# Performance work log

Hardware: AMD Instinct MI355X
Metric: run time of the kernel (lower is better)

Reference implementation:

```python
import jax, jax.numpy as jnp
import numpy as np

DIMS = 512
NUM_HEADS = 8
KEY_DIM = DIMS // NUM_HEADS  # 64
VAL_DIM = DIMS               # 512, shared across heads
B, L = 4, 2048


def setup_inputs() -> dict:
    key = jax.random.key(0)
    ks = jax.random.split(key, 13)
    s = 0.02
    return {
        "query": jax.random.normal(ks[0], (B, L, DIMS), dtype=jnp.float32),
        "key": jax.random.normal(ks[1], (B, L, DIMS), dtype=jnp.float32),
        "value": jax.random.normal(ks[2], (B, L, DIMS), dtype=jnp.float32),
        # linear weights stored as (in, out)
        "Wq": jax.random.normal(ks[3], (DIMS, KEY_DIM * NUM_HEADS), dtype=jnp.float32) * s,
        "bq": jnp.zeros((KEY_DIM * NUM_HEADS,), dtype=jnp.float32),
        "Wk": jax.random.normal(ks[4], (DIMS, KEY_DIM * NUM_HEADS), dtype=jnp.float32) * s,
        "bk": jnp.zeros((KEY_DIM * NUM_HEADS,), dtype=jnp.float32),
        "Wv": jax.random.normal(ks[5], (DIMS, VAL_DIM), dtype=jnp.float32) * s,
        "bv": jnp.zeros((VAL_DIM,), dtype=jnp.float32),
        "Wo": jax.random.normal(ks[6], (VAL_DIM * NUM_HEADS, DIMS), dtype=jnp.float32) * s,
        "bo": jnp.zeros((DIMS,), dtype=jnp.float32),
    }


def reference(query, key, value, Wq, bq, Wk, bk, Wv, bv, Wo, bo):
    b, l, _ = query.shape
    m = key.shape[1]
    q = (query @ Wq + bq).reshape(b, l, KEY_DIM, NUM_HEADS)   # blkh
    k = (key @ Wk + bk).reshape(b, m, KEY_DIM, NUM_HEADS)     # bmkh
    v = value @ Wv + bv                                        # bmv (shared over heads)
    # causal mask: -inf strictly above the diagonal
    mask = jnp.where(jnp.arange(m)[None, :] > jnp.arange(l)[:, None],
                     jnp.float32(-jnp.inf), jnp.float32(0.0))  # [l, m]
    scores = jnp.einsum('blkh,bmkh->bhlm', q, k) + mask
    # original divides (scores+mask) by sqrt(key_dim) before softmax
    attn = jax.nn.softmax(scores / jnp.sqrt(jnp.float32(KEY_DIM)), axis=-1)
    vals = jnp.einsum('bhlm,bmv->blhv', attn, v).reshape(b, l, NUM_HEADS * VAL_DIM)
    return vals @ Wo + bo
```

## Files before the change

kernel.cpp:

```cpp
#include <hip/hip_runtime.h>
#include <hip/hip_bf16.h>


typedef __attribute__((ext_vector_type(8))) short bf16x8;
typedef __attribute__((ext_vector_type(4))) float f32x4;
typedef unsigned short u16;
typedef unsigned int u32;

#define DIMS  512
#define NHEAD 8
#define KDIM  64
#define VDIM  512
#define BATCH 4
#define SEQ   2048
#define ROWS  (BATCH * SEQ)
#define OCOLS (NHEAD * VDIM)

__device__ __forceinline__ u16 f2bf(float x) {
  __hip_bfloat16 b = __float2bfloat16(x);
  u16 u; __builtin_memcpy(&u, &b, 2); return u;
}

__global__ __launch_bounds__(256) void cast_bf16(
    const float* __restrict__ in, u16* __restrict__ out, int n8) {
  int i = blockIdx.x * 256 + threadIdx.x;
  if (i >= n8) return;
  const float4* p = reinterpret_cast<const float4*>(in) + (size_t)i * 2;
  float4 a0 = p[0], a1 = p[1];
  bf16x8 v;
  v[0] = f2bf(a0.x); v[1] = f2bf(a0.y); v[2] = f2bf(a0.z); v[3] = f2bf(a0.w);
  v[4] = f2bf(a1.x); v[5] = f2bf(a1.y); v[6] = f2bf(a1.z); v[7] = f2bf(a1.w);
  reinterpret_cast<bf16x8*>(out)[i] = v;
}

__global__ __launch_bounds__(256) void transpose_to_bf16(
    const float* __restrict__ in, u16* __restrict__ out, int R, int C) {
  __shared__ float t[32][33];
  int tx = threadIdx.x & 31, ty = threadIdx.x >> 5;
  int r0 = blockIdx.y * 32, c0 = blockIdx.x * 32;
  #pragma unroll
  for (int i = 0; i < 32; i += 8)
    t[ty + i][tx] = in[(size_t)(r0 + ty + i) * C + c0 + tx];
  __syncthreads();
  #pragma unroll
  for (int i = 0; i < 32; i += 8) {
    int oc = ty + i;
    out[(size_t)(c0 + oc) * R + r0 + tx] = f2bf(t[tx][oc]);
  }
}

__global__ __launch_bounds__(256) void proj_kernel(
    const u16* __restrict__ Xb, const u16* __restrict__ Wt,
    const float* __restrict__ bias, u16* __restrict__ out,
    int mode, float scale) {
  __shared__ u16 Ct[64][72];
  int lane = threadIdx.x & 63, wave = threadIdx.x >> 6;
  int g = lane >> 4, l15 = lane & 15;
  int row0 = blockIdx.y * 64, cb = blockIdx.x * 64;
  int gr = row0 + wave * 16 + l15;
  f32x4 acc[4] = {};
  for (int k0 = 0; k0 < DIMS; k0 += 32) {
    int ka = k0 + g * 8;
    bf16x8 a = *reinterpret_cast<const bf16x8*>(Xb + (size_t)gr * DIMS + ka);
    #pragma unroll
    for (int c = 0; c < 4; ++c) {
      bf16x8 bfr = *reinterpret_cast<const bf16x8*>(Wt + (size_t)(cb + c * 16 + l15) * DIMS + ka);
      acc[c] = __builtin_amdgcn_mfma_f32_16x16x32_bf16(a, bfr, acc[c], 0, 0, 0);
    }
  }
  #pragma unroll
  for (int c = 0; c < 4; ++c) {
    int col = c * 16 + l15;
    float bi = bias[cb + col];
    #pragma unroll
    for (int r = 0; r < 4; ++r) {
      int rl = wave * 16 + g * 4 + r;
      float v = (acc[c][r] + bi) * scale;
      if (mode == 0) Ct[rl][col] = f2bf(v);
      else           Ct[col][rl] = f2bf(v);
    }
  }
  __syncthreads();
  if (mode == 0) {
    int kd0 = cb >> 3;
    #pragma unroll
    for (int s2 = 0; s2 < 2; ++s2) {
      int seg = threadIdx.x + s2 * 256;
      int l = seg >> 3, h = seg & 7;
      bf16x8 vp;
      #pragma unroll
      for (int j = 0; j < 8; ++j) vp[j] = (short)Ct[l][h + 8 * j];
      int row = row0 + l;
      int b = row >> 11, ll = row & 2047;
      *reinterpret_cast<bf16x8*>(out + (((size_t)(b * NHEAD + h) * SEQ + ll) * KDIM + kd0)) = vp;
    }
  } else {
    int v_ = threadIdx.x >> 2, ch = threadIdx.x & 3;
    int b = row0 >> 11, m0 = row0 & 2047;
    bf16x8 p0, p1;
    #pragma unroll
    for (int j = 0; j < 8; ++j) { p0[j] = (short)Ct[v_][ch * 16 + j]; p1[j] = (short)Ct[v_][ch * 16 + 8 + j]; }
    u16* dst = out + ((size_t)(b * VDIM + cb + v_)) * SEQ + m0 + ch * 16;
    *reinterpret_cast<bf16x8*>(dst) = p0;
    *reinterpret_cast<bf16x8*>(dst + 8) = p1;
  }
}

__global__ __launch_bounds__(256, 3) void attn_kernel(
    const u16* __restrict__ Qp, const u16* __restrict__ Kp,
    const u16* __restrict__ Vt, u16* __restrict__ vals) {
  __shared__ u16 Plds[2][32 * 64];
  __shared__ float Lpart[4][32];
  __shared__ float Rinv[32];
  int lane = threadIdx.x & 63, wave = threadIdx.x >> 6;
  int g = lane >> 4, l15 = lane & 15;
  int wg = blockIdx.x;
  int xcd = wg & 7, idx = wg >> 3;
  int bh = xcd * 4 + (idx & 3);
  int qt = 63 - (idx >> 2);
  int b = bh >> 3, h = bh & 7;
  int q0 = qt * 32;
  const u16* Qh = Qp + (size_t)bh * SEQ * KDIM;
  const u16* Kh = Kp + (size_t)bh * SEQ * KDIM;
  const u16* Vw = Vt + (size_t)b * VDIM * SEQ + (size_t)(wave * 128) * SEQ;

  bf16x8 qa[2][2];
  #pragma unroll
  for (int rf = 0; rf < 2; ++rf)
    #pragma unroll
    for (int ks = 0; ks < 2; ++ks)
      qa[rf][ks] = *reinterpret_cast<const bf16x8*>(
          Qh + (size_t)(q0 + rf * 16 + l15) * KDIM + ks * 32 + g * 8);

  f32x4 acc[2][8] = {};
  float rs[2][4] = {};
  int nt = (qt >> 1) + 1;
  int pcol = wave * 16 + l15;

  auto kload = [&](int t, bf16x8* kb) {
    const u16* base = Kh + (size_t)(t * 64 + wave * 16 + l15) * KDIM;
    kb[0] = *reinterpret_cast<const bf16x8*>(base + g * 8);
    kb[1] = *reinterpret_cast<const bf16x8*>(base + 32 + g * 8);
  };
  auto sphase = [&](int t, bf16x8 kb0, bf16x8 kb1) {
    int m0 = t * 64;
    u16* P = Plds[t & 1];
    f32x4 s[2] = {};
    #pragma unroll
    for (int rf = 0; rf < 2; ++rf) {
      s[rf] = __builtin_amdgcn_mfma_f32_16x16x32_bf16(qa[rf][0], kb0, s[rf], 0, 0, 0);
      s[rf] = __builtin_amdgcn_mfma_f32_16x16x32_bf16(qa[rf][1], kb1, s[rf], 0, 0, 0);
    }
    #pragma unroll
    for (int rf = 0; rf < 2; ++rf)
      #pragma unroll
      for (int r = 0; r < 4; ++r) {
        int prow = rf * 16 + g * 4 + r;
        float p = (m0 + pcol > q0 + prow) ? 0.f : exp2f(s[rf][r]);
        rs[rf][r] += p;
        P[prow * 64 + (pcol ^ ((prow & 7) << 3))] = f2bf(p);
      }
  };

  { bf16x8 kb[2]; kload(0, kb); sphase(0, kb[0], kb[1]); }
  __syncthreads();

  for (int t = 0; t < nt; ++t) {
    int m0 = t * 64;
    const u16* P = Plds[t & 1];
    bool more = (t + 1 < nt);
    bf16x8 kb[2];
    if (more) kload(t + 1, kb);
    #pragma unroll
    for (int ks = 0; ks < 2; ++ks) {
      bf16x8 vb[8];
      #pragma unroll
      for (int c = 0; c < 8; ++c)
        vb[c] = *reinterpret_cast<const bf16x8*>(
            Vw + (size_t)(c * 16 + l15) * SEQ + m0 + ks * 32 + g * 8);
      bf16x8 pa[2];
      #pragma unroll
      for (int ar = 0; ar < 2; ++ar) {
        int qr = ar * 16 + l15;
        pa[ar] = *reinterpret_cast<const bf16x8*>(
            &P[qr * 64 + ((ks * 32 + g * 8) ^ ((qr & 7) << 3))]);
      }
      #pragma unroll
      for (int c = 0; c < 8; ++c)
        #pragma unroll
        for (int ar = 0; ar < 2; ++ar)
          acc[ar][c] = __builtin_amdgcn_mfma_f32_16x16x32_bf16(pa[ar], vb[c], acc[ar][c], 0, 0, 0);
    }
    if (more) sphase(t + 1, kb[0], kb[1]);
    __syncthreads();
  }

  #pragma unroll
  for (int rf = 0; rf < 2; ++rf)
    #pragma unroll
    for (int r = 0; r < 4; ++r) {
      float v = rs[rf][r];
      v += __shfl_xor(v, 1); v += __shfl_xor(v, 2);
      v += __shfl_xor(v, 4); v += __shfl_xor(v, 8);
      rs[rf][r] = v;
    }
  if (l15 == 0) {
    #pragma unroll
    for (int rf = 0; rf < 2; ++rf)
      #pragma unroll
      for (int r = 0; r < 4; ++r)
        Lpart[wave][rf * 16 + g * 4 + r] = rs[rf][r];
  }
  __syncthreads();
  if (threadIdx.x < 32)
    Rinv[threadIdx.x] = 1.0f / (Lpart[0][threadIdx.x] + Lpart[1][threadIdx.x] +
                                Lpart[2][threadIdx.x] + Lpart[3][threadIdx.x]);
  __syncthreads();

  #pragma unroll
  for (int ar = 0; ar < 2; ++ar) {
    #pragma unroll
    for (int c = 0; c < 8; ++c) {
      int vcol = wave * 128 + c * 16 + l15;
      #pragma unroll
      for (int r = 0; r < 4; ++r) {
        int row = ar * 16 + g * 4 + r;
        float o = acc[ar][c][r] * Rinv[row];
        vals[((size_t)(b * SEQ + q0 + row)) * OCOLS + h * VDIM + vcol] = f2bf(o);
      }
    }
  }
}

__global__ __launch_bounds__(256) void out_gemm(
    const u16* __restrict__ vals, const u16* __restrict__ Wot,
    const float* __restrict__ bo, float* __restrict__ out) {
  __shared__ char As[128 * 128];
  __shared__ char Bs[64 * 128];
  int t = threadIdx.x;
  int lane = t & 63, wave = t >> 6;
  int g = lane >> 4, l15 = lane & 15;
  int id = (blockIdx.x & 7) * 64 + (blockIdx.x >> 3);
  int bx = id & 7, by = id >> 3;
  int row0 = by * 128, col0 = bx * 64;
  const int NT = OCOLS / 64;

  auto aglob = [&](int kt, int i) {
    int cid = t + i * 256, r = cid >> 3, ch = cid & 7;
    return *reinterpret_cast<const bf16x8*>(vals + (size_t)(row0 + r) * OCOLS + kt * 64 + ch * 8);
  };
  auto bglob = [&](int kt, int i) {
    int cid = t + i * 256, r = cid >> 3, ch = cid & 7;
    return *reinterpret_cast<const bf16x8*>(Wot + (size_t)(col0 + r) * OCOLS + kt * 64 + ch * 8);
  };
  auto stash = [&](bf16x8* av, bf16x8* bv) {
    #pragma unroll
    for (int i = 0; i < 4; ++i) {
      int cid = t + i * 256, r = cid >> 3, ch = cid & 7;
      *reinterpret_cast<bf16x8*>(As + r * 128 + ((ch * 16) ^ ((r & 7) << 4))) = av[i];
    }
    #pragma unroll
    for (int i = 0; i < 2; ++i) {
      int cid = t + i * 256, r = cid >> 3, ch = cid & 7;
      *reinterpret_cast<bf16x8*>(Bs + r * 128 + ((ch * 16) ^ ((r & 7) << 4))) = bv[i];
    }
  };

  f32x4 acc[2][4] = {};
  bf16x8 av[4], bv[2];
  #pragma unroll
  for (int i = 0; i < 4; ++i) av[i] = aglob(0, i);
  #pragma unroll
  for (int i = 0; i < 2; ++i) bv[i] = bglob(0, i);
  stash(av, bv);
  __syncthreads();

  for (int kt = 0; kt < NT; ++kt) {
    bf16x8 an[4], bn[2];
    if (kt + 1 < NT) {
      #pragma unroll
      for (int i = 0; i < 4; ++i) an[i] = aglob(kt + 1, i);
      #pragma unroll
      for (int i = 0; i < 2; ++i) bn[i] = bglob(kt + 1, i);
    }
    #pragma unroll
    for (int ks = 0; ks < 2; ++ks) {
      bf16x8 af[2];
      #pragma unroll
      for (int rf = 0; rf < 2; ++rf) {
        int row = wave * 32 + rf * 16 + l15;
        af[rf] = *reinterpret_cast<const bf16x8*>(As + row * 128 + ((ks * 64 + g * 16) ^ ((row & 7) << 4)));
      }
      #pragma unroll
      for (int c = 0; c < 4; ++c) {
        int row = c * 16 + l15;
        bf16x8 bfr = *reinterpret_cast<const bf16x8*>(Bs + row * 128 + ((ks * 64 + g * 16) ^ ((row & 7) << 4)));
        #pragma unroll
        for (int rf = 0; rf < 2; ++rf)
          acc[rf][c] = __builtin_amdgcn_mfma_f32_16x16x32_bf16(af[rf], bfr, acc[rf][c], 0, 0, 0);
      }
    }
    __syncthreads();
    if (kt + 1 < NT) {
      stash(an, bn);
      __syncthreads();
    }
  }

  #pragma unroll
  for (int c = 0; c < 4; ++c) {
    int col = col0 + c * 16 + l15;
    float bi = bo[col];
    #pragma unroll
    for (int rf = 0; rf < 2; ++rf)
      #pragma unroll
      for (int r = 0; r < 4; ++r) {
        int row = row0 + wave * 32 + rf * 16 + g * 4 + r;
        out[(size_t)row * DIMS + col] = acc[rf][c][r] + bi;
      }
  }
}

extern "C" void kernel_launch(void* const* d_in, const int* in_sizes, int n_in,
                              void* d_out, int out_size, void* d_ws, size_t ws_size,
                              hipStream_t stream) {
  const float* query = (const float*)d_in[0];
  const float* key   = (const float*)d_in[1];
  const float* value = (const float*)d_in[2];
  const float* Wq    = (const float*)d_in[3];
  const float* bq    = (const float*)d_in[4];
  const float* Wk    = (const float*)d_in[5];
  const float* bk    = (const float*)d_in[6];
  const float* Wv    = (const float*)d_in[7];
  const float* bv    = (const float*)d_in[8];
  const float* Wo    = (const float*)d_in[9];
  const float* bo    = (const float*)d_in[10];
  float* out = (float*)d_out;

  char* ws = (char*)d_ws;
  size_t off = 0;
  auto alloc = [&](size_t bytes) {
    char* p = ws + off; off += (bytes + 255) & ~(size_t)255; return p;
  };
  u16* Wqt  = (u16*)alloc((size_t)512 * 512 * 2);
  u16* Wkt  = (u16*)alloc((size_t)512 * 512 * 2);
  u16* Wvt  = (u16*)alloc((size_t)512 * 512 * 2);
  u16* Wot  = (u16*)alloc((size_t)512 * 4096 * 2);
  u16* Qp   = (u16*)alloc((size_t)BATCH * NHEAD * SEQ * KDIM * 2);
  u16* Kp   = (u16*)alloc((size_t)BATCH * NHEAD * SEQ * KDIM * 2);
  u16* Vt   = (u16*)alloc((size_t)BATCH * VDIM * SEQ * 2);
  u16* vals = (u16*)alloc((size_t)ROWS * OCOLS * 2);
  u16* Xq = vals;
  u16* Xk = vals + (size_t)ROWS * DIMS;
  u16* Xv = vals + (size_t)2 * ROWS * DIMS;

  dim3 tb(256);
  const int N8 = ROWS * DIMS / 8;
  cast_bf16<<<dim3(N8 / 256), tb, 0, stream>>>(query, Xq, N8);
  cast_bf16<<<dim3(N8 / 256), tb, 0, stream>>>(key,   Xk, N8);
  cast_bf16<<<dim3(N8 / 256), tb, 0, stream>>>(value, Xv, N8);

  transpose_to_bf16<<<dim3(16, 16), tb, 0, stream>>>(Wq, Wqt, 512, 512);
  transpose_to_bf16<<<dim3(16, 16), tb, 0, stream>>>(Wk, Wkt, 512, 512);
  transpose_to_bf16<<<dim3(16, 16), tb, 0, stream>>>(Wv, Wvt, 512, 512);
  transpose_to_bf16<<<dim3(16, 128), tb, 0, stream>>>(Wo, Wot, 4096, 512);

  const float qscale = 0.18033688011112042f;
  proj_kernel<<<dim3(8, 128), tb, 0, stream>>>(Xq, Wqt, bq, Qp, 0, qscale);
  proj_kernel<<<dim3(8, 128), tb, 0, stream>>>(Xk, Wkt, bk, Kp, 0, 1.0f);
  proj_kernel<<<dim3(8, 128), tb, 0, stream>>>(Xv, Wvt, bv, Vt, 2, 1.0f);

  attn_kernel<<<dim3(2048), tb, 0, stream>>>(Qp, Kp, Vt, vals);

  out_gemm<<<dim3(512), tb, 0, stream>>>(vals, Wot, bo, out);
}
```

Measured before the change: 604.6 us.

## Widen attention workgroup to 8 waves with 128-key tiles and transposed score MFMA

The attention kernel now runs 512 threads (8 waves), each covering 64 value columns instead of 128, and processes 128 keys per iteration instead of 64. Scores are computed as K·Q^T, so each lane owns one query row and can write four packed bf16 probabilities in one store and keep a single row-sum. Key sub-tiles lying entirely above the causal diagonal on the last tile are zero-filled without doing the MFMA. The aim is fewer loop iterations and barriers, higher occupancy, and less per-lane reduction work. The cost is more LDS per block and partly wasted work on the padded final tile.

```diff
diff --git a/kernel.cpp b/kernel.cpp
--- a/kernel.cpp
+++ b/kernel.cpp
@@ -106,11 +106,11 @@
   }
 }
 
-__global__ __launch_bounds__(256, 3) void attn_kernel(
+__global__ __launch_bounds__(512, 4) void attn_kernel(
     const u16* __restrict__ Qp, const u16* __restrict__ Kp,
     const u16* __restrict__ Vt, u16* __restrict__ vals) {
-  __shared__ u16 Plds[2][32 * 64];
-  __shared__ float Lpart[4][32];
+  __shared__ u16 Plds[2][32 * 128];
+  __shared__ float Lpart[8][32];
   __shared__ float Rinv[32];
   int lane = threadIdx.x & 63, wave = threadIdx.x >> 6;
   int g = lane >> 4, l15 = lane & 15;
@@ -122,71 +122,88 @@
   int q0 = qt * 32;
   const u16* Qh = Qp + (size_t)bh * SEQ * KDIM;
   const u16* Kh = Kp + (size_t)bh * SEQ * KDIM;
-  const u16* Vw = Vt + (size_t)b * VDIM * SEQ + (size_t)(wave * 128) * SEQ;
-
-  bf16x8 qa[2][2];
+  const u16* Vw = Vt + (size_t)b * VDIM * SEQ + (size_t)(wave * 64) * SEQ;
+
+  bf16x8 qb[2][2];
   #pragma unroll
   for (int rf = 0; rf < 2; ++rf)
     #pragma unroll
     for (int ks = 0; ks < 2; ++ks)
-      qa[rf][ks] = *reinterpret_cast<const bf16x8*>(
+      qb[rf][ks] = *reinterpret_cast<const bf16x8*>(
           Qh + (size_t)(q0 + rf * 16 + l15) * KDIM + ks * 32 + g * 8);
 
-  f32x4 acc[2][8] = {};
-  float rs[2][4] = {};
-  int nt = (qt >> 1) + 1;
-  int pcol = wave * 16 + l15;
+  f32x4 acc[2][4] = {};
+  float rs[2] = {0.f, 0.f};
+  int nt = ((q0 + 31) >> 7) + 1;
+  int mrow = wave * 16 + l15;
 
   auto kload = [&](int t, bf16x8* kb) {
-    const u16* base = Kh + (size_t)(t * 64 + wave * 16 + l15) * KDIM;
+    const u16* base = Kh + (size_t)(t * 128 + mrow) * KDIM;
     kb[0] = *reinterpret_cast<const bf16x8*>(base + g * 8);
     kb[1] = *reinterpret_cast<const bf16x8*>(base + 32 + g * 8);
   };
   auto sphase = [&](int t, bf16x8 kb0, bf16x8 kb1) {
-    int m0 = t * 64;
     u16* P = Plds[t & 1];
-    f32x4 s[2] = {};
+    int mbase = t * 128 + wave * 16;
+    bool lastt = (t == nt - 1);
+    if (lastt && (mbase > q0 + 31)) {
+      #pragma unroll
+      for (int rf = 0; rf < 2; ++rf) {
+        int ql = rf * 16 + l15;
+        uint2 z; z.x = 0u; z.y = 0u;
+        *reinterpret_cast<uint2*>(&P[ql * 128 + ((wave * 16 + g * 4) ^ ((ql & 7) << 3))]) = z;
+      }
+      return;
+    }
+    f32x4 st[2] = {};
     #pragma unroll
     for (int rf = 0; rf < 2; ++rf) {
-      s[rf] = __builtin_amdgcn_mfma_f32_16x16x32_bf16(qa[rf][0], kb0, s[rf], 0, 0, 0);
-      s[rf] = __builtin_amdgcn_mfma_f32_16x16x32_bf16(qa[rf][1], kb1, s[rf], 0, 0, 0);
-    }
-    #pragma unroll
-    for (int rf = 0; rf < 2; ++rf)
+      st[rf] = __builtin_amdgcn_mfma_f32_16x16x32_bf16(kb0, qb[rf][0], st[rf], 0, 0, 0);
+      st[rf] = __builtin_amdgcn_mfma_f32_16x16x32_bf16(kb1, qb[rf][1], st[rf], 0, 0, 0);
+    }
+    #pragma unroll
+    for (int rf = 0; rf < 2; ++rf) {
+      int qg = q0 + rf * 16 + l15;
+      u16 pb[4];
       #pragma unroll
       for (int r = 0; r < 4; ++r) {
-        int prow = rf * 16 + g * 4 + r;
-        float p = (m0 + pcol > q0 + prow) ? 0.f : exp2f(s[rf][r]);
-        rs[rf][r] += p;
-        P[prow * 64 + (pcol ^ ((prow & 7) << 3))] = f2bf(p);
-      }
+        float p = (lastt && (mbase + g * 4 + r > qg)) ? 0.f : exp2f(st[rf][r]);
+        pb[r] = f2bf(p);
+        rs[rf] += p;
+      }
+      uint2 w;
+      w.x = (u32)pb[0] | ((u32)pb[1] << 16);
+      w.y = (u32)pb[2] | ((u32)pb[3] << 16);
+      int ql = rf * 16 + l15;
+      *reinterpret_cast<uint2*>(&P[ql * 128 + ((wave * 16 + g * 4) ^ ((ql & 7) << 3))]) = w;
+    }
   };
 
   { bf16x8 kb[2]; kload(0, kb); sphase(0, kb[0], kb[1]); }
   __syncthreads();
 
   for (int t = 0; t < nt; ++t) {
-    int m0 = t * 64;
+    int m0 = t * 128;
     const u16* P = Plds[t & 1];
     bool more = (t + 1 < nt);
     bf16x8 kb[2];
     if (more) kload(t + 1, kb);
     #pragma unroll
-    for (int ks = 0; ks < 2; ++ks) {
-      bf16x8 vb[8];
-      #pragma unroll
-      for (int c = 0; c < 8; ++c)
+    for (int ks = 0; ks < 4; ++ks) {
+      bf16x8 vb[4];
+      #pragma unroll
+      for (int c = 0; c < 4; ++c)
         vb[c] = *reinterpret_cast<const bf16x8*>(
             Vw + (size_t)(c * 16 + l15) * SEQ + m0 + ks * 32 + g * 8);
       bf16x8 pa[2];
       #pragma unroll
       for (int ar = 0; ar < 2; ++ar) {
-        int qr = ar * 16 + l15;
+        int ql = ar * 16 + l15;
         pa[ar] = *reinterpret_cast<const bf16x8*>(
-            &P[qr * 64 + ((ks * 32 + g * 8) ^ ((qr & 7) << 3))]);
-      }
-      #pragma unroll
-      for (int c = 0; c < 8; ++c)
+            &P[ql * 128 + ((ks * 32 + g * 8) ^ ((ql & 7) << 3))]);
+      }
+      #pragma unroll
+      for (int c = 0; c < 4; ++c)
         #pragma unroll
         for (int ar = 0; ar < 2; ++ar)
           acc[ar][c] = __builtin_amdgcn_mfma_f32_16x16x32_bf16(pa[ar], vb[c], acc[ar][c], 0, 0, 0);
@@ -196,32 +213,30 @@
   }
 
   #pragma unroll
-  for (int rf = 0; rf < 2; ++rf)
-    #pragma unroll
-    for (int r = 0; r < 4; ++r) {
-      float v = rs[rf][r];
-      v += __shfl_xor(v, 1); v += __shfl_xor(v, 2);
-      v += __shfl_xor(v, 4); v += __shfl_xor(v, 8);
-      rs[rf][r] = v;
-    }
-  if (l15 == 0) {
-    #pragma unroll
-    for (int rf = 0; rf < 2; ++rf)
-      #pragma unroll
-      for (int r = 0; r < 4; ++r)
-        Lpart[wave][rf * 16 + g * 4 + r] = rs[rf][r];
-  }
-  __syncthreads();
-  if (threadIdx.x < 32)
-    Rinv[threadIdx.x] = 1.0f / (Lpart[0][threadIdx.x] + Lpart[1][threadIdx.x] +
-                                Lpart[2][threadIdx.x] + Lpart[3][threadIdx.x]);
+  for (int rf = 0; rf < 2; ++rf) {
+    float v = rs[rf];
+    v += __shfl_xor(v, 16);
+    v += __shfl_xor(v, 32);
+    rs[rf] = v;
+  }
+  if (lane < 16) {
+    Lpart[wave][lane] = rs[0];
+    Lpart[wave][16 + lane] = rs[1];
+  }
+  __syncthreads();
+  if (threadIdx.x < 32) {
+    float s = 0.f;
+    #pragma unroll
+    for (int w = 0; w < 8; ++w) s += Lpart[w][threadIdx.x];
+    Rinv[threadIdx.x] = 1.0f / s;
+  }
   __syncthreads();
 
   #pragma unroll
   for (int ar = 0; ar < 2; ++ar) {
     #pragma unroll
-    for (int c = 0; c < 8; ++c) {
-      int vcol = wave * 128 + c * 16 + l15;
+    for (int c = 0; c < 4; ++c) {
+      int vcol = wave * 64 + c * 16 + l15;
       #pragma unroll
       for (int r = 0; r < 4; ++r) {
         int row = ar * 16 + g * 4 + r;
@@ -370,7 +385,7 @@
   proj_kernel<<<dim3(8, 128), tb, 0, stream>>>(Xk, Wkt, bk, Kp, 0, 1.0f);
   proj_kernel<<<dim3(8, 128), tb, 0, stream>>>(Xv, Wvt, bv, Vt, 2, 1.0f);
 
-  attn_kernel<<<dim3(2048), tb, 0, stream>>>(Qp, Kp, Vt, vals);
+  attn_kernel<<<dim3(2048), dim3(512), 0, stream>>>(Qp, Kp, Vt, vals);
 
   out_gemm<<<dim3(512), tb, 0, stream>>>(vals, Wot, bo, out);
 }
```

New measurement: 590.5 us. -2.3%, faster.
